# Optimization experiments

Hardware: AMD Instinct MI355X
Metric: run time of the kernel (lower is better)

## Reference

```python
import jax, jax.numpy as jnp
import numpy as np

N_HEADS = 16


def setup_inputs() -> dict:
    key = jax.random.key(0)
    ks = jax.random.split(key, 8)
    B, T, D = 2, 2048, 1024
    hd, rank = D // N_HEADS, 32
    std = 0.02
    inp = {
        "x": jax.random.normal(ks[0], (B, T, D), jnp.float32),
        "Wq": jax.random.normal(ks[1], (D, D), jnp.float32) * std,
        "bq": jnp.zeros((D,), jnp.float32),
        "Wk": jax.random.normal(ks[2], (D, D), jnp.float32) * std,
        "bk": jnp.zeros((D,), jnp.float32),
        "Wv": jax.random.normal(ks[3], (D, D), jnp.float32) * std,
        "bv": jnp.zeros((D,), jnp.float32),
        "Wo": jax.random.normal(ks[4], (D, D), jnp.float32) * std,
        "bo": jnp.zeros((D,), jnp.float32),
        # orthogonal-ish init via QR, matching nn.init.orthogonal_
        "U": jnp.linalg.qr(jax.random.normal(ks[5], (hd, rank), jnp.float32))[0],
        "V": jnp.linalg.qr(jax.random.normal(ks[6], (hd, rank), jnp.float32))[0],
    }
    return inp


def reference(x, Wq, bq, Wk, bk, Wv, bv, Wo, bo, U, V):
    B, T, D = x.shape
    H = N_HEADS
    hd = D // H
    rank = V.shape[1]
    # torch Linear: y = x @ W.T + b
    q = (x @ Wq.T + bq).reshape(B, T, H, hd).transpose(0, 2, 1, 3)  # [B,H,T,hd]
    k = (x @ Wk.T + bk).reshape(B, T, H, hd).transpose(0, 2, 1, 3)
    v = (x @ Wv.T + bv).reshape(B, T, H, hd).transpose(0, 2, 1, 3)
    # low-rank subspace projection (shared V across heads)
    zq = q @ V  # [B,H,T,rank]
    zk = k @ V
    zv = v @ V
    att = jnp.einsum("bhqr,bhkr->bhqk", zq, zk) / jnp.sqrt(jnp.float32(max(rank, 1)))
    att = jax.nn.softmax(att, axis=-1)
    y_r = jnp.einsum("bhqk,bhkr->bhqr", att, zv)  # [B,H,T,rank]
    y = y_r @ U.T  # reconstruct to [B,H,T,hd]
    y = y.transpose(0, 2, 1, 3).reshape(B, T, D)
    return y @ Wo.T + bo
```

## Files before the change

kernel.cpp:

```cpp
#include <hip/hip_runtime.h>
#include <hip/hip_bf16.h>
#include <cstdint>

#define NB 2
#define NT 2048
#define ND 1024
#define NH 16
#define HD 64
#define RANK 32
#define HR 512
#define ZSTR 1024

typedef _Float16 f16;
typedef _Float16 f16x2 __attribute__((ext_vector_type(2)));
typedef _Float16 f16x4 __attribute__((ext_vector_type(4)));
typedef _Float16 f16x8 __attribute__((ext_vector_type(8)));
typedef float f32x4 __attribute__((ext_vector_type(4)));

#define ZQ_SCALE 0.2550696805f

__device__ __forceinline__ float fast_exp2(float x) {
#if __has_builtin(__builtin_amdgcn_exp2f)
  return __builtin_amdgcn_exp2f(x);
#else
  return exp2f(x);
#endif
}

__global__ __launch_bounds__(256) void conv_f16(const float* __restrict__ in,
                                                f16* __restrict__ out, int n8) {
  int i = blockIdx.x * 256 + threadIdx.x;
  if (i >= n8) return;
  const float4* p = (const float4*)in + (size_t)i * 2;
  float4 a = p[0], b = p[1];
  f16x8 h = {(f16)a.x, (f16)a.y, (f16)a.z, (f16)a.w,
             (f16)b.x, (f16)b.y, (f16)b.z, (f16)b.w};
  *(f16x8*)(out + (size_t)i * 8) = h;
}

__global__ __launch_bounds__(256) void prep_wp(
    const float* __restrict__ Wq, const float* __restrict__ Wk,
    const float* __restrict__ Wv, const float* __restrict__ V,
    f16* __restrict__ Oq, f16* __restrict__ Ok, f16* __restrict__ Ov)
{
  __shared__ float Vs[HD][RANK];
  const int tid = threadIdx.x;
  const int Dp  = blockIdx.x * 256 + tid;
  const int h   = blockIdx.y;
  const int m   = blockIdx.z;
  const float* W = m == 0 ? Wq : m == 1 ? Wk : Wv;
  f16*         O = m == 0 ? Oq : m == 1 ? Ok : Ov;
  const float scale = m == 0 ? ZQ_SCALE : 1.0f;

  for (int i = tid; i < HD * RANK; i += 256) Vs[i >> 5][i & 31] = V[i];
  __syncthreads();

  float acc[RANK] = {};
#pragma unroll 4
  for (int d = 0; d < HD; ++d) {
    float w = W[(size_t)(h * HD + d) * ND + Dp];
#pragma unroll
    for (int r = 0; r < RANK; ++r) acc[r] = fmaf(w, Vs[d][r], acc[r]);
  }
#pragma unroll
  for (int r = 0; r < RANK; ++r)
    O[(size_t)(h * RANK + r) * ND + Dp] = (f16)(acc[r] * scale);
}

__global__ __launch_bounds__(512) void prep_bp(
    const float* __restrict__ bq, const float* __restrict__ bk,
    const float* __restrict__ bv, const float* __restrict__ V,
    float* __restrict__ bqp, float* __restrict__ bkp, float* __restrict__ bvp)
{
  const int m  = blockIdx.x;
  const int hr = threadIdx.x;
  const float* bs = m == 0 ? bq : m == 1 ? bk : bv;
  float*       o  = m == 0 ? bqp : m == 1 ? bkp : bvp;
  const int h = hr >> 5, r = hr & 31;
  float a = 0.f;
#pragma unroll
  for (int d = 0; d < HD; ++d) a = fmaf(bs[h * HD + d], V[d * RANK + r], a);
  o[hr] = a * (m == 0 ? ZQ_SCALE : 1.0f);
}

__global__ __launch_bounds__(256) void prep_wo(
    const float* __restrict__ Wo, const float* __restrict__ U,
    f16* __restrict__ WoPP)
{
  __shared__ float Ws[64][65];
  __shared__ float Us[HD][RANK];
  const int tid = threadIdx.x;
  const int n0  = blockIdx.x * 64;
  const int h   = blockIdx.y;

  for (int i = tid; i < HD * RANK; i += 256) Us[i >> 5][i & 31] = U[i];
#pragma unroll
  for (int it = 0; it < 16; ++it) {
    int idx = it * 256 + tid;
    int i = idx >> 6, d = idx & 63;
    Ws[i][d] = Wo[(size_t)(n0 + i) * ND + h * HD + d];
  }
  __syncthreads();

  const int i  = tid >> 2;
  const int r0 = (tid & 3) << 3;
  float acc[8] = {};
#pragma unroll 4
  for (int d = 0; d < HD; ++d) {
    float w = Ws[i][d];
#pragma unroll
    for (int j = 0; j < 8; ++j) acc[j] = fmaf(w, Us[d][r0 + j], acc[j]);
  }
  f16x8 o = {(f16)acc[0], (f16)acc[1], (f16)acc[2], (f16)acc[3],
             (f16)acc[4], (f16)acc[5], (f16)acc[6], (f16)acc[7]};
  *(f16x8*)(WoPP + (size_t)(n0 + i) * HR + h * RANK + r0) = o;
}

#define GBM 128
#define GBN 64
#define GBK 64

__device__ __forceinline__ int swz(int b) { return b ^ (((b >> 7) & 7) << 4); }

__device__ __forceinline__ void gload16(const f16* g, const f16* lds_wave_base) {
  __builtin_amdgcn_global_load_lds(
      (const __attribute__((address_space(1))) void*)g,
      (__attribute__((address_space(3))) void*)lds_wave_base, 16, 0, 0);
}

template <typename OT, bool ROWBIAS>
__global__ __launch_bounds__(256) void gemm_f16_bias(
    const f16* __restrict__ A, const f16* __restrict__ W,
    const float* __restrict__ bias, OT* __restrict__ C, int M, int N, int K)
{
  __shared__ f16 sA[GBM * GBK];
  __shared__ f16 sB[GBN * GBK];
  const int tid  = threadIdx.x;
  const int wid  = tid >> 6;
  const int lane = tid & 63;
  const int bm = blockIdx.x * GBM;
  const int bn = blockIdx.y * GBN;
  const int wm = (wid >> 1) * 64;
  const int wn = (wid & 1) * 32;

  f32x4 acc[4][2];
#pragma unroll
  for (int i = 0; i < 4; ++i)
#pragma unroll
    for (int j = 0; j < 2; ++j) acc[i][j] = (f32x4){0.f, 0.f, 0.f, 0.f};

  int arow[4], aoff[4];
#pragma unroll
  for (int i = 0; i < 4; ++i) {
    int Lg = swz(i * 4096 + tid * 16);
    arow[i] = Lg >> 7;
    aoff[i] = (Lg & 127) >> 1;
  }
  int brow[2], boff[2];
#pragma unroll
  for (int i = 0; i < 2; ++i) {
    int Lg = swz(i * 4096 + tid * 16);
    brow[i] = Lg >> 7;
    boff[i] = (Lg & 127) >> 1;
  }

  const char* sAc = (const char*)sA;
  const char* sBc = (const char*)sB;

  for (int k0 = 0; k0 < K; k0 += GBK) {
    __syncthreads();
#pragma unroll
    for (int i = 0; i < 4; ++i)
      gload16(A + (size_t)(bm + arow[i]) * K + k0 + aoff[i],
              (const f16*)((const char*)sA + i * 4096 + wid * 1024));
#pragma unroll
    for (int i = 0; i < 2; ++i)
      gload16(W + (size_t)(bn + brow[i]) * K + k0 + boff[i],
              (const f16*)((const char*)sB + i * 4096 + wid * 1024));
    __syncthreads();

#pragma unroll
    for (int kh = 0; kh < 2; ++kh) {
      const int kb = kh * 64 + ((lane >> 4) << 4);
      f16x8 af[4], bf[2];
#pragma unroll
      for (int mi = 0; mi < 4; ++mi) {
        int Lg = (wm + mi * 16 + (lane & 15)) * 128 + kb;
        af[mi] = *(const f16x8*)(sAc + swz(Lg));
      }
#pragma unroll
      for (int ni = 0; ni < 2; ++ni) {
        int Lg = (wn + ni * 16 + (lane & 15)) * 128 + kb;
        bf[ni] = *(const f16x8*)(sBc + swz(Lg));
      }
#pragma unroll
      for (int mi = 0; mi < 4; ++mi)
#pragma unroll
        for (int ni = 0; ni < 2; ++ni)
          acc[mi][ni] = __builtin_amdgcn_mfma_f32_16x16x32_f16(
              af[mi], bf[ni], acc[mi][ni], 0, 0, 0);
    }
  }

  const int cl = lane & 15, rh = lane >> 4;
#pragma unroll
  for (int ni = 0; ni < 2; ++ni) {
    const int col = bn + wn + ni * 16 + cl;
    const float cb = ROWBIAS ? 0.f : bias[col];
#pragma unroll
    for (int mi = 0; mi < 4; ++mi) {
      const int r0 = bm + wm + mi * 16 + rh * 4;
#pragma unroll
      for (int r = 0; r < 4; ++r) {
        const float bb = ROWBIAS ? bias[r0 + r] : cb;
        C[(size_t)(r0 + r) * N + col] = (OT)(acc[mi][ni][r] + bb);
      }
    }
  }
}

#define QBLK 64
#define KBLK 64
#define SKLD 40

__global__ __launch_bounds__(256) void attn_mfma(
    const f16* __restrict__ zqk,
    const f16* __restrict__ zvT,
    f16* __restrict__ y_rh)
{
  __shared__ f16 sK[KBLK * SKLD];
  __shared__ f16 sVT[RANK * KBLK];
  __shared__ f16 sP[4][16 * KBLK];
  __shared__ float sL[4][16];

  const int tid  = threadIdx.x;
  const int wid  = tid >> 6;
  const int lane = tid & 63;
  const int g    = lane >> 4;
  const int m16  = lane & 15;
  const int bh   = blockIdx.y;
  const int b    = bh >> 4;
  const int h    = bh & 15;
  const int q0   = blockIdx.x * QBLK + wid * 16;

  const f16* zqb = zqk + (size_t)b * NT * ZSTR + h * RANK;
  const f16* zkb = zqk + (size_t)b * NT * ZSTR + HR + h * RANK;
  const char* zvb = (const char*)zvT;

  f16x8 qfrag = *(const f16x8*)(zqb + (size_t)(q0 + m16) * ZSTR + g * 8);

  const int zk_row = tid >> 2, zk_c = tid & 3;
  const int zv_r = tid >> 3;
  const int zv_srcoff = ((tid & 7) * 16) ^ ((zv_r & 7) << 4);
  const size_t zv_rowbase = ((size_t)(h * RANK + zv_r) * NB + b) * (NT * 2);

  f32x4 acc0 = {0.f, 0.f, 0.f, 0.f}, acc1 = {0.f, 0.f, 0.f, 0.f};
  float lpart = 0.f;

  char* sPw = (char*)&sP[wid][0];
  char* sVTc = (char*)sVT;
  const int swzq = (m16 & 7) << 4;

  for (int k0 = 0; k0 < NT; k0 += KBLK) {
    f16x8 kreg = *(const f16x8*)(zkb + (size_t)(k0 + zk_row) * ZSTR + zk_c * 8);
    __syncthreads();
    __builtin_amdgcn_global_load_lds(
        (const __attribute__((address_space(1))) void*)(
            zvb + zv_rowbase + k0 * 2 + zv_srcoff),
        (__attribute__((address_space(3))) void*)(sVTc + wid * 1024), 16, 0, 0);
    *(f16x8*)(sK + zk_row * SKLD + zk_c * 8) = kreg;
    __syncthreads();

    f32x4 s[4];
#pragma unroll
    for (int kt = 0; kt < 4; ++kt) {
      f16x8 kf = *(const f16x8*)(sK + (kt * 16 + m16) * SKLD + g * 8);
      f32x4 z4 = {0.f, 0.f, 0.f, 0.f};
      s[kt] = __builtin_amdgcn_mfma_f32_16x16x32_f16(kf, qfrag, z4, 0, 0, 0);
    }

#pragma unroll
    for (int kt = 0; kt < 4; ++kt) {
      float p0 = fast_exp2(s[kt][0]);
      float p1 = fast_exp2(s[kt][1]);
      float p2 = fast_exp2(s[kt][2]);
      float p3 = fast_exp2(s[kt][3]);
      lpart += (p0 + p1) + (p2 + p3);
      f16x4 pk = {(f16)p0, (f16)p1, (f16)p2, (f16)p3};
      *(f16x4*)(sPw + m16 * 128 + ((kt * 32 + g * 8) ^ swzq)) = pk;
    }

#pragma unroll
    for (int kt2 = 0; kt2 < 2; ++kt2) {
      const int rb = kt2 * 64 + g * 16;
      f16x8 pf = *(const f16x8*)(sPw + m16 * 128 + (rb ^ swzq));
      f16x8 v0 = *(const f16x8*)(sVTc + m16 * 128 + (rb ^ swzq));
      f16x8 v1 = *(const f16x8*)(sVTc + (16 + m16) * 128 + (rb ^ swzq));
      acc0 = __builtin_amdgcn_mfma_f32_16x16x32_f16(pf, v0, acc0, 0, 0, 0);
      acc1 = __builtin_amdgcn_mfma_f32_16x16x32_f16(pf, v1, acc1, 0, 0, 0);
    }
  }

  lpart += __shfl_xor(lpart, 16);
  lpart += __shfl_xor(lpart, 32);
  if (lane < 16) sL[wid][lane] = lpart;
  __syncthreads();

  f16* yb = y_rh + ((size_t)(b * NT) + q0) * HR + h * RANK;
#pragma unroll
  for (int r = 0; r < 4; ++r) {
    const float inv = 1.f / sL[wid][g * 4 + r];
    yb[(size_t)(g * 4 + r) * HR + m16]      = (f16)(acc0[r] * inv);
    yb[(size_t)(g * 4 + r) * HR + 16 + m16] = (f16)(acc1[r] * inv);
  }
}

extern "C" void kernel_launch(void* const* d_in, const int* in_sizes, int n_in,
                              void* d_out, int out_size, void* d_ws, size_t ws_size,
                              hipStream_t stream) {
  const float* x  = (const float*)d_in[0];
  const float* Wq = (const float*)d_in[1];
  const float* bq = (const float*)d_in[2];
  const float* Wk = (const float*)d_in[3];
  const float* bk = (const float*)d_in[4];
  const float* Wv = (const float*)d_in[5];
  const float* bv = (const float*)d_in[6];
  const float* Wo = (const float*)d_in[7];
  const float* bo = (const float*)d_in[8];
  const float* U  = (const float*)d_in[9];
  const float* V  = (const float*)d_in[10];
  float* out = (float*)d_out;

  float* ws = (float*)d_ws;
  f16*   x_h   = (f16*)(ws + 0);
  f16*   WqkPT = (f16*)(ws + 2097152);
  f16*   WvPT  = (f16*)(ws + 2621440);
  f16*   WoPP  = (f16*)(ws + 2883584);
  float* bqkp  = ws + 3145728;
  float* bvp   = ws + 3146752;
  f16*   zqk   = (f16*)(ws + 3147264);
  f16*   zvT   = (f16*)(ws + 5244416);
  f16*   y_rh  = (f16*)(ws + 6292992);

  conv_f16<<<2048, 256, 0, stream>>>(x, x_h, 524288);

  prep_wp<<<dim3(4, 16, 3), 256, 0, stream>>>(
      Wq, Wk, Wv, V, WqkPT, WqkPT + 512 * 1024, WvPT);
  prep_bp<<<3, 512, 0, stream>>>(bq, bk, bv, V, bqkp, bqkp + 512, bvp);
  prep_wo<<<dim3(16, 16), 256, 0, stream>>>(Wo, U, WoPP);

  gemm_f16_bias<f16, false><<<dim3(32, 16), 256, 0, stream>>>(
      x_h, WqkPT, bqkp, zqk, NB * NT, ZSTR, ND);
  gemm_f16_bias<f16, true><<<dim3(4, 64), 256, 0, stream>>>(
      WvPT, x_h, bvp, zvT, HR, NB * NT, ND);

  dim3 ga(NT / QBLK, NB * NH);
  attn_mfma<<<ga, 256, 0, stream>>>(zqk, zvT, y_rh);

  gemm_f16_bias<float, false><<<dim3(32, 16), 256, 0, stream>>>(
      y_rh, WoPP, bo, out, NB * NT, ND, HR);
}
```

Measured before the change: 198.7 us.

## Enlarge GEMM N-tile and attention query block, fold bias prep into weight prep

Raises the GEMM block tile from 128x64 to 128x128, so each wave computes a 64x64 sub-tile with 4x4 MFMA accumulators and reuses A fragments across more columns. Doubles the attention query block so each wave handles two 16-row query groups against each loaded K/V tile, halving K/V reloads per query. Merges the bias-projection kernel into prep_wp to remove one launch. The cost is fewer blocks in flight (grids halve) and higher register and LDS use per block, which may cut occupancy.

```diff
diff --git a/kernel.cpp b/kernel.cpp
--- a/kernel.cpp
+++ b/kernel.cpp
@@ -41,7 +41,10 @@
 __global__ __launch_bounds__(256) void prep_wp(
     const float* __restrict__ Wq, const float* __restrict__ Wk,
     const float* __restrict__ Wv, const float* __restrict__ V,
-    f16* __restrict__ Oq, f16* __restrict__ Ok, f16* __restrict__ Ov)
+    const float* __restrict__ bq, const float* __restrict__ bk,
+    const float* __restrict__ bv,
+    f16* __restrict__ Oq, f16* __restrict__ Ok, f16* __restrict__ Ov,
+    float* __restrict__ bqp, float* __restrict__ bkp, float* __restrict__ bvp)
 {
   __shared__ float Vs[HD][RANK];
   const int tid = threadIdx.x;
@@ -65,22 +68,15 @@
 #pragma unroll
   for (int r = 0; r < RANK; ++r)
     O[(size_t)(h * RANK + r) * ND + Dp] = (f16)(acc[r] * scale);
-}
-
-__global__ __launch_bounds__(512) void prep_bp(
-    const float* __restrict__ bq, const float* __restrict__ bk,
-    const float* __restrict__ bv, const float* __restrict__ V,
-    float* __restrict__ bqp, float* __restrict__ bkp, float* __restrict__ bvp)
-{
-  const int m  = blockIdx.x;
-  const int hr = threadIdx.x;
-  const float* bs = m == 0 ? bq : m == 1 ? bk : bv;
-  float*       o  = m == 0 ? bqp : m == 1 ? bkp : bvp;
-  const int h = hr >> 5, r = hr & 31;
-  float a = 0.f;
-#pragma unroll
-  for (int d = 0; d < HD; ++d) a = fmaf(bs[h * HD + d], V[d * RANK + r], a);
-  o[hr] = a * (m == 0 ? ZQ_SCALE : 1.0f);
+
+  if (blockIdx.x == 0 && tid < RANK) {
+    const float* bs = m == 0 ? bq : m == 1 ? bk : bv;
+    float*       o  = m == 0 ? bqp : m == 1 ? bkp : bvp;
+    float a = 0.f;
+#pragma unroll
+    for (int d = 0; d < HD; ++d) a = fmaf(bs[h * HD + d], Vs[d][tid], a);
+    o[h * RANK + tid] = a * scale;
+  }
 }
 
 __global__ __launch_bounds__(256) void prep_wo(
@@ -117,7 +113,7 @@
 }
 
 #define GBM 128
-#define GBN 64
+#define GBN 128
 #define GBK 64
 
 __device__ __forceinline__ int swz(int b) { return b ^ (((b >> 7) & 7) << 4); }
@@ -141,27 +137,20 @@
   const int bm = blockIdx.x * GBM;
   const int bn = blockIdx.y * GBN;
   const int wm = (wid >> 1) * 64;
-  const int wn = (wid & 1) * 32;
-
-  f32x4 acc[4][2];
+  const int wn = (wid & 1) * 64;
+
+  f32x4 acc[4][4];
 #pragma unroll
   for (int i = 0; i < 4; ++i)
 #pragma unroll
-    for (int j = 0; j < 2; ++j) acc[i][j] = (f32x4){0.f, 0.f, 0.f, 0.f};
-
-  int arow[4], aoff[4];
+    for (int j = 0; j < 4; ++j) acc[i][j] = (f32x4){0.f, 0.f, 0.f, 0.f};
+
+  int grow[4], goff[4];
 #pragma unroll
   for (int i = 0; i < 4; ++i) {
     int Lg = swz(i * 4096 + tid * 16);
-    arow[i] = Lg >> 7;
-    aoff[i] = (Lg & 127) >> 1;
-  }
-  int brow[2], boff[2];
-#pragma unroll
-  for (int i = 0; i < 2; ++i) {
-    int Lg = swz(i * 4096 + tid * 16);
-    brow[i] = Lg >> 7;
-    boff[i] = (Lg & 127) >> 1;
+    grow[i] = Lg >> 7;
+    goff[i] = (Lg & 127) >> 1;
   }
 
   const char* sAc = (const char*)sA;
@@ -171,32 +160,32 @@
     __syncthreads();
 #pragma unroll
     for (int i = 0; i < 4; ++i)
-      gload16(A + (size_t)(bm + arow[i]) * K + k0 + aoff[i],
+      gload16(A + (size_t)(bm + grow[i]) * K + k0 + goff[i],
               (const f16*)((const char*)sA + i * 4096 + wid * 1024));
 #pragma unroll
-    for (int i = 0; i < 2; ++i)
-      gload16(W + (size_t)(bn + brow[i]) * K + k0 + boff[i],
+    for (int i = 0; i < 4; ++i)
+      gload16(W + (size_t)(bn + grow[i]) * K + k0 + goff[i],
               (const f16*)((const char*)sB + i * 4096 + wid * 1024));
     __syncthreads();
 
 #pragma unroll
     for (int kh = 0; kh < 2; ++kh) {
       const int kb = kh * 64 + ((lane >> 4) << 4);
-      f16x8 af[4], bf[2];
+      f16x8 af[4], bf[4];
 #pragma unroll
       for (int mi = 0; mi < 4; ++mi) {
         int Lg = (wm + mi * 16 + (lane & 15)) * 128 + kb;
         af[mi] = *(const f16x8*)(sAc + swz(Lg));
       }
 #pragma unroll
-      for (int ni = 0; ni < 2; ++ni) {
+      for (int ni = 0; ni < 4; ++ni) {
         int Lg = (wn + ni * 16 + (lane & 15)) * 128 + kb;
         bf[ni] = *(const f16x8*)(sBc + swz(Lg));
       }
 #pragma unroll
       for (int mi = 0; mi < 4; ++mi)
 #pragma unroll
-        for (int ni = 0; ni < 2; ++ni)
+        for (int ni = 0; ni < 4; ++ni)
           acc[mi][ni] = __builtin_amdgcn_mfma_f32_16x16x32_f16(
               af[mi], bf[ni], acc[mi][ni], 0, 0, 0);
     }
@@ -204,7 +193,7 @@
 
   const int cl = lane & 15, rh = lane >> 4;
 #pragma unroll
-  for (int ni = 0; ni < 2; ++ni) {
+  for (int ni = 0; ni < 4; ++ni) {
     const int col = bn + wn + ni * 16 + cl;
     const float cb = ROWBIAS ? 0.f : bias[col];
 #pragma unroll
@@ -219,7 +208,7 @@
   }
 }
 
-#define QBLK 64
+#define QBLK 128
 #define KBLK 64
 #define SKLD 40
 
@@ -230,8 +219,8 @@
 {
   __shared__ f16 sK[KBLK * SKLD];
   __shared__ f16 sVT[RANK * KBLK];
-  __shared__ f16 sP[4][16 * KBLK];
-  __shared__ float sL[4][16];
+  __shared__ f16 sP[4][32 * KBLK];
+  __shared__ float sL[4][32];
 
   const int tid  = threadIdx.x;
   const int wid  = tid >> 6;
@@ -241,21 +230,23 @@
   const int bh   = blockIdx.y;
   const int b    = bh >> 4;
   const int h    = bh & 15;
-  const int q0   = blockIdx.x * QBLK + wid * 16;
+  const int q0   = blockIdx.x * QBLK + wid * 32;
 
   const f16* zqb = zqk + (size_t)b * NT * ZSTR + h * RANK;
-  const f16* zkb = zqk + (size_t)b * NT * ZSTR + HR + h * RANK;
+  const f16* zkb = zqb + HR;
   const char* zvb = (const char*)zvT;
 
-  f16x8 qfrag = *(const f16x8*)(zqb + (size_t)(q0 + m16) * ZSTR + g * 8);
+  f16x8 qfA = *(const f16x8*)(zqb + (size_t)(q0 + m16) * ZSTR + g * 8);
+  f16x8 qfB = *(const f16x8*)(zqb + (size_t)(q0 + 16 + m16) * ZSTR + g * 8);
 
   const int zk_row = tid >> 2, zk_c = tid & 3;
   const int zv_r = tid >> 3;
   const int zv_srcoff = ((tid & 7) * 16) ^ ((zv_r & 7) << 4);
   const size_t zv_rowbase = ((size_t)(h * RANK + zv_r) * NB + b) * (NT * 2);
 
-  f32x4 acc0 = {0.f, 0.f, 0.f, 0.f}, acc1 = {0.f, 0.f, 0.f, 0.f};
-  float lpart = 0.f;
+  f32x4 aA0 = {0.f, 0.f, 0.f, 0.f}, aA1 = {0.f, 0.f, 0.f, 0.f};
+  f32x4 aB0 = {0.f, 0.f, 0.f, 0.f}, aB1 = {0.f, 0.f, 0.f, 0.f};
+  float lA = 0.f, lB = 0.f;
 
   char* sPw = (char*)&sP[wid][0];
   char* sVTc = (char*)sVT;
@@ -271,47 +262,60 @@
     *(f16x8*)(sK + zk_row * SKLD + zk_c * 8) = kreg;
     __syncthreads();
 
-    f32x4 s[4];
 #pragma unroll
     for (int kt = 0; kt < 4; ++kt) {
       f16x8 kf = *(const f16x8*)(sK + (kt * 16 + m16) * SKLD + g * 8);
       f32x4 z4 = {0.f, 0.f, 0.f, 0.f};
-      s[kt] = __builtin_amdgcn_mfma_f32_16x16x32_f16(kf, qfrag, z4, 0, 0, 0);
+      f32x4 sa = __builtin_amdgcn_mfma_f32_16x16x32_f16(kf, qfA, z4, 0, 0, 0);
+      f32x4 sb = __builtin_amdgcn_mfma_f32_16x16x32_f16(kf, qfB, z4, 0, 0, 0);
+      float a0 = fast_exp2(sa[0]), a1 = fast_exp2(sa[1]);
+      float a2 = fast_exp2(sa[2]), a3 = fast_exp2(sa[3]);
+      float b0 = fast_exp2(sb[0]), b1 = fast_exp2(sb[1]);
+      float b2 = fast_exp2(sb[2]), b3 = fast_exp2(sb[3]);
+      lA += (a0 + a1) + (a2 + a3);
+      lB += (b0 + b1) + (b2 + b3);
+      const int off = (kt * 32 + g * 8) ^ swzq;
+      f16x4 pa = {(f16)a0, (f16)a1, (f16)a2, (f16)a3};
+      f16x4 pb = {(f16)b0, (f16)b1, (f16)b2, (f16)b3};
+      *(f16x4*)(sPw + m16 * 128 + off)        = pa;
+      *(f16x4*)(sPw + (16 + m16) * 128 + off) = pb;
     }
 
 #pragma unroll
-    for (int kt = 0; kt < 4; ++kt) {
-      float p0 = fast_exp2(s[kt][0]);
-      float p1 = fast_exp2(s[kt][1]);
-      float p2 = fast_exp2(s[kt][2]);
-      float p3 = fast_exp2(s[kt][3]);
-      lpart += (p0 + p1) + (p2 + p3);
-      f16x4 pk = {(f16)p0, (f16)p1, (f16)p2, (f16)p3};
-      *(f16x4*)(sPw + m16 * 128 + ((kt * 32 + g * 8) ^ swzq)) = pk;
+    for (int kt2 = 0; kt2 < 2; ++kt2) {
+      const int rb = (kt2 * 64 + g * 16) ^ swzq;
+      f16x8 pfA = *(const f16x8*)(sPw + m16 * 128 + rb);
+      f16x8 pfB = *(const f16x8*)(sPw + (16 + m16) * 128 + rb);
+      f16x8 v0 = *(const f16x8*)(sVTc + m16 * 128 + rb);
+      f16x8 v1 = *(const f16x8*)(sVTc + (16 + m16) * 128 + rb);
+      aA0 = __builtin_amdgcn_mfma_f32_16x16x32_f16(pfA, v0, aA0, 0, 0, 0);
+      aA1 = __builtin_amdgcn_mfma_f32_16x16x32_f16(pfA, v1, aA1, 0, 0, 0);
+      aB0 = __builtin_amdgcn_mfma_f32_16x16x32_f16(pfB, v0, aB0, 0, 0, 0);
+      aB1 = __builtin_amdgcn_mfma_f32_16x16x32_f16(pfB, v1, aB1, 0, 0, 0);
     }
-
-#pragma unroll
-    for (int kt2 = 0; kt2 < 2; ++kt2) {
-      const int rb = kt2 * 64 + g * 16;
-      f16x8 pf = *(const f16x8*)(sPw + m16 * 128 + (rb ^ swzq));
-      f16x8 v0 = *(const f16x8*)(sVTc + m16 * 128 + (rb ^ swzq));
-      f16x8 v1 = *(const f16x8*)(sVTc + (16 + m16) * 128 + (rb ^ swzq));
-      acc0 = __builtin_amdgcn_mfma_f32_16x16x32_f16(pf, v0, acc0, 0, 0, 0);
-      acc1 = __builtin_amdgcn_mfma_f32_16x16x32_f16(pf, v1, acc1, 0, 0, 0);
-    }
-  }
-
-  lpart += __shfl_xor(lpart, 16);
-  lpart += __shfl_xor(lpart, 32);
-  if (lane < 16) sL[wid][lane] = lpart;
+  }
+
+  lA += __shfl_xor(lA, 16);
+  lA += __shfl_xor(lA, 32);
+  lB += __shfl_xor(lB, 16);
+  lB += __shfl_xor(lB, 32);
+  if (lane < 16) {
+    sL[wid][lane]      = lA;
+    sL[wid][16 + lane] = lB;
+  }
   __syncthreads();
 
   f16* yb = y_rh + ((size_t)(b * NT) + q0) * HR + h * RANK;
 #pragma unroll
   for (int r = 0; r < 4; ++r) {
-    const float inv = 1.f / sL[wid][g * 4 + r];
-    yb[(size_t)(g * 4 + r) * HR + m16]      = (f16)(acc0[r] * inv);
-    yb[(size_t)(g * 4 + r) * HR + 16 + m16] = (f16)(acc1[r] * inv);
+    const int qa = g * 4 + r;
+    const float invA = 1.f / sL[wid][qa];
+    yb[(size_t)qa * HR + m16]      = (f16)(aA0[r] * invA);
+    yb[(size_t)qa * HR + 16 + m16] = (f16)(aA1[r] * invA);
+    const int qb2 = 16 + qa;
+    const float invB = 1.f / sL[wid][qb2];
+    yb[(size_t)qb2 * HR + m16]      = (f16)(aB0[r] * invB);
+    yb[(size_t)qb2 * HR + 16 + m16] = (f16)(aB1[r] * invB);
   }
 }
 
@@ -345,18 +349,18 @@
   conv_f16<<<2048, 256, 0, stream>>>(x, x_h, 524288);
 
   prep_wp<<<dim3(4, 16, 3), 256, 0, stream>>>(
-      Wq, Wk, Wv, V, WqkPT, WqkPT + 512 * 1024, WvPT);
-  prep_bp<<<3, 512, 0, stream>>>(bq, bk, bv, V, bqkp, bqkp + 512, bvp);
+      Wq, Wk, Wv, V, bq, bk, bv,
+      WqkPT, WqkPT + 512 * 1024, WvPT, bqkp, bqkp + 512, bvp);
   prep_wo<<<dim3(16, 16), 256, 0, stream>>>(Wo, U, WoPP);
 
-  gemm_f16_bias<f16, false><<<dim3(32, 16), 256, 0, stream>>>(
+  gemm_f16_bias<f16, false><<<dim3(32, 8), 256, 0, stream>>>(
       x_h, WqkPT, bqkp, zqk, NB * NT, ZSTR, ND);
-  gemm_f16_bias<f16, true><<<dim3(4, 64), 256, 0, stream>>>(
+  gemm_f16_bias<f16, true><<<dim3(4, 32), 256, 0, stream>>>(
       WvPT, x_h, bvp, zvT, HR, NB * NT, ND);
 
   dim3 ga(NT / QBLK, NB * NH);
   attn_mfma<<<ga, 256, 0, stream>>>(zqk, zvT, y_rh);
 
-  gemm_f16_bias<float, false><<<dim3(32, 16), 256, 0, stream>>>(
+  gemm_f16_bias<float, false><<<dim3(32, 8), 256, 0, stream>>>(
       y_rh, WoPP, bo, out, NB * NT, ND, HR);
 }
```

Result: slower. 212.9 us (+7.2%).
